# Optimization experiments

Measured on AMD Instinct MI355X. Metric: run time of the kernel, lower is better.

The kernel has to match this reference:

```python
import jax, jax.numpy as jnp
import numpy as np

T, H, O, L = 8192, 512, 256, 5  # num_frames, hidden(=input), output, num_layers


def setup_inputs() -> dict:
    key = jax.random.key(0)
    ks = jax.random.split(key, 16)
    s = 1.0 / np.sqrt(H)
    def w(k, shape):
        return jax.random.uniform(k, shape, jnp.float32, -s, s)
    d = {"x": jax.random.normal(ks[0], (T, H), jnp.float32)}
    names = ["Wz", "Uz", "Wr", "Ur", "Wh", "Uh"]
    for i, n in enumerate(names):
        d[n] = w(ks[1 + i], (L, H, H))
        d["b" + n] = w(ks[7 + i], (L, H))
    d["fcW"] = w(ks[13], (O, H))
    d["fcb"] = w(ks[14], (O,))
    return d


def _gru_forward(x, Wz, Uz, Wr, Ur, Wh, Uh, bWz, bUz, bWr, bUr, bWh, bUh):
    # x: [T, H]; weights: [L, H, H]; biases: [L, H]
    nl, hs = Wz.shape[0], Wz.shape[1]
    h0 = jnp.zeros((nl, hs), x.dtype)

    def time_step(h, x_t):  # h: [L, H], x_t: [H]
        def layer_step(x_in, p):
            wz, uz, wr, ur, wh, uh, bwz, buz, bwr, bur, bwh, buh, h_prev = p
            z = jax.nn.sigmoid(x_in @ wz.T + bwz + h_prev @ uz.T + buz)
            r = jax.nn.sigmoid(x_in @ wr.T + bwr + h_prev @ ur.T + bur)
            h_tilde = jnp.tanh(x_in @ wh.T + bwh + (r * h_prev) @ uh.T + buh)
            h_new = (1.0 - z) * h_prev + z * h_tilde
            return h_new, h_new  # next layer's input is this layer's hidden

        _, h_new = jax.lax.scan(
            layer_step, x_t,
            (Wz, Uz, Wr, Ur, Wh, Uh, bWz, bUz, bWr, bUr, bWh, bUh, h))
        return h_new, h_new[-1]  # carry new stacked state, emit top-layer h

    h_final, outs = jax.lax.scan(time_step, h0, x)
    return outs, h_final  # outs: [T, H], h_final: [L, H]


def reference(x, Wz, Uz, Wr, Ur, Wh, Uh, bWz, bUz, bWr, bUr, bWh, bUh, fcW, fcb):
    outs, h_final = _gru_forward(x, Wz, Uz, Wr, Ur, Wh, Uh,
                                 bWz, bUz, bWr, bUr, bWh, bUh)
    out = outs @ fcW.T + fcb  # [T, O]
    return out, h_final
```

## Files before the change

kernel.cpp:

```cpp
#include <hip/hip_runtime.h>
#include <math.h>

#define TT 8192
#define HH 512
#define LL 5
#define OO 256
#define GG 32
#define NR 16
#define NTHR 256
#define RB 64
#define HOT 4u
#define CAP_TAG 2000000u
#define CAP_PRG 200000u

typedef unsigned long long u64;
typedef unsigned u32;


__device__ __forceinline__ float wred(float v) {
#pragma unroll
  for (int off = 32; off > 0; off >>= 1) v += __shfl_xor(v, off, 64);
  return v;
}

__device__ __forceinline__ float sigm(float v) {
  return 1.0f / (1.0f + expf(-v));
}

__device__ __forceinline__ u64 ldA(const u64* p) {
  return __hip_atomic_load((u64*)p, __ATOMIC_RELAXED, __HIP_MEMORY_SCOPE_AGENT);
}
__device__ __forceinline__ void stA(u64* p, u64 v) {
  __hip_atomic_store(p, v, __ATOMIC_RELAXED, __HIP_MEMORY_SCOPE_AGENT);
}
__device__ __forceinline__ u64 pack(u32 tag, float v) {
  return ((u64)tag << 32) | (u64)__float_as_uint(v);
}


__global__ void init_ws(u32* __restrict__ p, int n) {
  int stride = gridDim.x * blockDim.x;
  for (int i = blockIdx.x * blockDim.x + threadIdx.x; i < n; i += stride) p[i] = 0u;
}


__launch_bounds__(NTHR, 1)
__global__ void gru_pipeline(
    const float* __restrict__ x,
    const float* __restrict__ Wz, const float* __restrict__ bWz,
    const float* __restrict__ Uz, const float* __restrict__ bUz,
    const float* __restrict__ Wr, const float* __restrict__ bWr,
    const float* __restrict__ Ur, const float* __restrict__ bUr,
    const float* __restrict__ Wh, const float* __restrict__ bWh,
    const float* __restrict__ Uh, const float* __restrict__ bUh,
    u64* __restrict__ hring,
    u64* __restrict__ rring,
    float* __restrict__ htop,
    u32* __restrict__ prog,
    float* __restrict__ dout)
{
  const int blk = blockIdx.x;
  const int l = blk / GG;
  const int g = blk % GG;
  const bool ltop = (l == LL - 1);
  const int i0 = g * NR;

  const int tid = threadIdx.x;
  const int wave = tid >> 6;
  const int lane = tid & 63;
  const int j0 = lane * 8;
  const int j = tid * 2;

  __shared__ float xs[HH];
  __shared__ float hs[HH];
  __shared__ float rh[HH];
  __shared__ int dead_s;
  volatile int* dead = &dead_s;
  if (tid == 0) dead_s = 0;

  float wz[4][8], uz[4][8], wr[4][8], ur[4][8], wh[4][8], uh[4][8];
  float bz[4], br[4], bh[4];
  int rowg[4];
#pragma unroll
  for (int k = 0; k < 4; ++k) {
    const int i = i0 + wave + 4 * k;
    rowg[k] = i;
    const size_t ro = ((size_t)l * HH + i) * HH + j0;
    *(float4*)&wz[k][0] = *(const float4*)(Wz + ro);
    *(float4*)&wz[k][4] = *(const float4*)(Wz + ro + 4);
    *(float4*)&uz[k][0] = *(const float4*)(Uz + ro);
    *(float4*)&uz[k][4] = *(const float4*)(Uz + ro + 4);
    *(float4*)&wr[k][0] = *(const float4*)(Wr + ro);
    *(float4*)&wr[k][4] = *(const float4*)(Wr + ro + 4);
    *(float4*)&ur[k][0] = *(const float4*)(Ur + ro);
    *(float4*)&ur[k][4] = *(const float4*)(Ur + ro + 4);
    *(float4*)&wh[k][0] = *(const float4*)(Wh + ro);
    *(float4*)&wh[k][4] = *(const float4*)(Wh + ro + 4);
    *(float4*)&uh[k][0] = *(const float4*)(Uh + ro);
    *(float4*)&uh[k][4] = *(const float4*)(Uh + ro + 4);
    bz[k] = bWz[l * HH + i] + bUz[l * HH + i];
    br[k] = bWr[l * HH + i] + bUr[l * HH + i];
    bh[k] = bWh[l * HH + i] + bUh[l * HH + i];
  }

  u64* my_h = hring + (size_t)l * RB * HH;
  const u64* up_h = hring + (size_t)(l > 0 ? l - 1 : 0) * RB * HH;
  u64* my_r = rring + (size_t)l * 2 * HH;
  u32* my_prog = prog + l * GG + g;
  u32* dn_prog = prog + (l < LL - 1 ? l + 1 : l) * GG;

  float zreg[4], awreg[4], hpown[4];
#pragma unroll
  for (int k = 0; k < 4; ++k) { zreg[k] = 0.f; awreg[k] = 0.f; hpown[k] = 0.f; }

  __syncthreads();

  for (int t = 0; t < TT; ++t) {
    {
      const u64* sx = (l > 0) ? up_h + (size_t)(t & (RB - 1)) * HH + j : (const u64*)0;
      const u64* sh = (t > 0) ? my_h + (size_t)((t - 1) & (RB - 1)) * HH + j : (const u64*)0;
      const u32 tagx = (u32)(t + 1), tagh = (u32)t;
      u64 ax = 0, bx = 0, ah = 0, bh2 = 0;
      if (sx) { ax = ldA(sx); bx = ldA(sx + 1); }
      if (sh) { ah = ldA(sh); bh2 = ldA(sh + 1); }
      u32 n = 0;
      for (;;) {
        const bool badx = sx && (((u32)(ax >> 32) != tagx) || ((u32)(bx >> 32) != tagx));
        const bool badh = sh && (((u32)(ah >> 32) != tagh) || ((u32)(bh2 >> 32) != tagh));
        if (!badx && !badh) break;
        if (++n > HOT) {
          __builtin_amdgcn_s_sleep(2);
          if (*dead) break;
          if (n > CAP_TAG) { *dead = 1; break; }
        }
        if (badx) { ax = ldA(sx); bx = ldA(sx + 1); }
        if (badh) { ah = ldA(sh); bh2 = ldA(sh + 1); }
      }
      if (sx) { xs[j] = __uint_as_float((u32)ax); xs[j + 1] = __uint_as_float((u32)bx); }
      else {
        const float2 v = *(const float2*)&x[(size_t)t * HH + j];
        xs[j] = v.x; xs[j + 1] = v.y;
      }
      if (sh) { hs[j] = __uint_as_float((u32)ah); hs[j + 1] = __uint_as_float((u32)bh2); }
      else { hs[j] = 0.f; hs[j + 1] = 0.f; }
    }
    if (wave == 3 && !ltop && t >= RB && lane < GG) {
      const u32 need = (u32)(t - RB + 1);
      u32 n = 0;
      while (__hip_atomic_load(&dn_prog[lane], __ATOMIC_RELAXED,
                               __HIP_MEMORY_SCOPE_AGENT) < need) {
        if (*dead) break;
        if (++n > CAP_PRG) { *dead = 1; break; }
        __builtin_amdgcn_s_sleep(16);
      }
    }
    __syncthreads();

    if (tid == 0)
      __hip_atomic_store(my_prog, (u32)(t + 1), __ATOMIC_RELAXED, __HIP_MEMORY_SCOPE_AGENT);

    float xv[8], hv[8];
    *(float4*)&xv[0] = *(const float4*)&xs[j0];
    *(float4*)&xv[4] = *(const float4*)&xs[j0 + 4];
    *(float4*)&hv[0] = *(const float4*)&hs[j0];
    *(float4*)&hv[4] = *(const float4*)&hs[j0 + 4];
#pragma unroll
    for (int k = 0; k < 4; ++k) hpown[k] = hs[rowg[k]];

    u64* hsl = my_h + (size_t)(t & (RB - 1)) * HH;

    if (t == 0) {
#pragma unroll
      for (int k = 0; k < 4; ++k) {
        float az = 0.f, aw = 0.f;
#pragma unroll
        for (int q = 0; q < 8; ++q) {
          az = fmaf(wz[k][q], xv[q], az);
          aw = fmaf(wh[k][q], xv[q], aw);
        }
        az = wred(az); aw = wred(aw);
        if (lane == 0) {
          const float hnew = sigm(az + bz[k]) * tanhf(aw + bh[k]);
          stA(&hsl[rowg[k]], pack(1u, hnew));
          if (ltop) htop[(size_t)0 * HH + rowg[k]] = hnew;
        }
      }
      __syncthreads();
      continue;
    }

    u64* rs = my_r + (size_t)(t & 1) * HH;
    const u32 tag1 = (u32)(t + 1);
#pragma unroll
    for (int k = 0; k < 4; ++k) {
      float ar = 0.f;
#pragma unroll
      for (int q = 0; q < 8; ++q) {
        ar = fmaf(wr[k][q], xv[q], ar);
        ar = fmaf(ur[k][q], hv[q], ar);
      }
      ar = wred(ar);
      if (lane == 0) stA(&rs[rowg[k]], pack(tag1, sigm(ar + br[k])));
    }

#pragma unroll
    for (int k = 0; k < 4; ++k) {
      float az = 0.f, aw = 0.f;
#pragma unroll
      for (int q = 0; q < 8; ++q) {
        az = fmaf(wz[k][q], xv[q], az);
        az = fmaf(uz[k][q], hv[q], az);
        aw = fmaf(wh[k][q], xv[q], aw);
      }
      az = wred(az); aw = wred(aw);
      if (lane == 0) {
        zreg[k] = sigm(az + bz[k]);
        awreg[k] = aw + bh[k];
      }
    }

    {
      const u64* s = rs + j;
      u64 a = ldA(s), b = ldA(s + 1);
      u32 n = 0;
      while ((u32)(a >> 32) != tag1 || (u32)(b >> 32) != tag1) {
        if (++n > HOT) {
          __builtin_amdgcn_s_sleep(2);
          if (*dead) break;
          if (n > CAP_TAG) { *dead = 1; break; }
        }
        if ((u32)(a >> 32) != tag1) a = ldA(s);
        if ((u32)(b >> 32) != tag1) b = ldA(s + 1);
      }
      rh[j]     = __uint_as_float((u32)a) * hs[j];
      rh[j + 1] = __uint_as_float((u32)b) * hs[j + 1];
    }
    __syncthreads();

    float rhv[8];
    *(float4*)&rhv[0] = *(const float4*)&rh[j0];
    *(float4*)&rhv[4] = *(const float4*)&rh[j0 + 4];

#pragma unroll
    for (int k = 0; k < 4; ++k) {
      float u = 0.f;
#pragma unroll
      for (int q = 0; q < 8; ++q) u = fmaf(uh[k][q], rhv[q], u);
      u = wred(u);
      if (lane == 0) {
        const float z = zreg[k];
        const float ht = tanhf(awreg[k] + u);
        const float hnew = (1.f - z) * hpown[k] + z * ht;
        stA(&hsl[rowg[k]], pack(tag1, hnew));
        if (ltop) htop[(size_t)t * HH + rowg[k]] = hnew;
        if (t == TT - 1) dout[(size_t)TT * OO + (size_t)l * HH + rowg[k]] = hnew;
      }
    }
  }
}


__launch_bounds__(256)
__global__ void fc_gemm(const float* __restrict__ A,
                        const float* __restrict__ W,
                        const float* __restrict__ bias,
                        float* __restrict__ C) {
  __shared__ float As[16][68];
  __shared__ float Ws[16][68];
  const int bm = blockIdx.x;
  const int bn = blockIdx.y;
  const int tid = threadIdx.x;
  const int tx = tid & 15;
  const int ty = tid >> 4;
  const int r = tid >> 2;
  const int kc = (tid & 3) * 4;
  float acc[4][4];
#pragma unroll
  for (int a = 0; a < 4; ++a)
#pragma unroll
    for (int b2 = 0; b2 < 4; ++b2) acc[a][b2] = 0.f;

  for (int k0 = 0; k0 < HH; k0 += 16) {
    const float4 a4 = *(const float4*)&A[(size_t)(bm * 64 + r) * HH + k0 + kc];
    const float4 w4 = *(const float4*)&W[(size_t)(bn * 64 + r) * HH + k0 + kc];
    __syncthreads();
    As[kc + 0][r] = a4.x; As[kc + 1][r] = a4.y; As[kc + 2][r] = a4.z; As[kc + 3][r] = a4.w;
    Ws[kc + 0][r] = w4.x; Ws[kc + 1][r] = w4.y; Ws[kc + 2][r] = w4.z; Ws[kc + 3][r] = w4.w;
    __syncthreads();
#pragma unroll
    for (int kk = 0; kk < 16; ++kk) {
      const float4 av = *(const float4*)&As[kk][ty * 4];
      const float4 wv = *(const float4*)&Ws[kk][tx * 4];
      const float avv[4] = {av.x, av.y, av.z, av.w};
      const float wvv[4] = {wv.x, wv.y, wv.z, wv.w};
#pragma unroll
      for (int a = 0; a < 4; ++a)
#pragma unroll
        for (int b2 = 0; b2 < 4; ++b2)
          acc[a][b2] = fmaf(avv[a], wvv[b2], acc[a][b2]);
    }
  }
#pragma unroll
  for (int a = 0; a < 4; ++a) {
    const int row = bm * 64 + ty * 4 + a;
#pragma unroll
    for (int b2 = 0; b2 < 4; ++b2) {
      const int col = bn * 64 + tx * 4 + b2;
      C[(size_t)row * OO + col] = acc[a][b2] + bias[col];
    }
  }
}


extern "C" void kernel_launch(void* const* d_in, const int* in_sizes, int n_in,
                              void* d_out, int out_size, void* d_ws, size_t ws_size,
                              hipStream_t stream) {
  const float* p[15];
  for (int i = 0; i < 15 && i < n_in; ++i) p[i] = (const float*)d_in[i];

  const float *x, *Wz, *bWz, *Uz, *bUz, *Wr, *bWr, *Ur, *bUr, *Wh, *bWh, *Uh, *bUh, *fcW, *fcb;
  x = p[0];
  if (in_sizes[2] == LL * HH) {
    Wz = p[1]; bWz = p[2]; Uz = p[3]; bUz = p[4];
    Wr = p[5]; bWr = p[6]; Ur = p[7]; bUr = p[8];
    Wh = p[9]; bWh = p[10]; Uh = p[11]; bUh = p[12];
  } else {
    Wz = p[1]; Uz = p[2]; Wr = p[3]; Ur = p[4]; Wh = p[5]; Uh = p[6];
    bWz = p[7]; bUz = p[8]; bWr = p[9]; bUr = p[10]; bWh = p[11]; bUh = p[12];
  }
  fcW = p[13]; fcb = p[14];

  u64* hring = (u64*)d_ws;
  u64* rring = hring + (size_t)LL * RB * HH;
  u32* prog = (u32*)(rring + (size_t)LL * 2 * HH);
  float* htop = (float*)(prog + (size_t)LL * GG);

  const int zero_u32 = (int)(((size_t)LL * RB * HH + (size_t)LL * 2 * HH) * 2 + LL * GG);
  init_ws<<<512, 256, 0, stream>>>((u32*)d_ws, zero_u32);

  gru_pipeline<<<LL * GG, NTHR, 0, stream>>>(
      x, Wz, bWz, Uz, bUz, Wr, bWr, Ur, bUr, Wh, bWh, Uh, bUh,
      hring, rring, htop, prog, (float*)d_out);

  fc_gemm<<<dim3(TT / 64, OO / 64), 256, 0, stream>>>(
      htop, fcW, fcb, (float*)d_out);
}
```

Before: 54.05 ms.

## Make each wave poll global rings directly and drop block-level barriers

Each wave now reads the tagged hidden-state and upper-layer values straight from the global rings with a strided per-lane layout, instead of staging them in shared memory behind __syncthreads. Progress counters are tracked per wave, and r*h_prev is computed by the owning lane before publishing, so consumers no longer multiply by h themselves. This removes two block barriers per timestep and the shared-memory round trip on the serial critical path. In exchange, every wave issues its own atomic polls, which multiplies global polling traffic.

```diff
diff --git a/kernel.cpp b/kernel.cpp
--- a/kernel.cpp
+++ b/kernel.cpp
@@ -6,12 +6,10 @@
 #define LL 5
 #define OO 256
 #define GG 32
-#define NR 16
 #define NTHR 256
 #define RB 64
-#define HOT 4u
-#define CAP_TAG 2000000u
-#define CAP_PRG 200000u
+#define CAP_TAG 4000000u
+#define CAP_PRG 4000000u
 
 typedef unsigned long long u64;
 typedef unsigned u32;
@@ -31,6 +29,12 @@
   return __hip_atomic_load((u64*)p, __ATOMIC_RELAXED, __HIP_MEMORY_SCOPE_AGENT);
 }
 __device__ __forceinline__ void stA(u64* p, u64 v) {
+  __hip_atomic_store(p, v, __ATOMIC_RELAXED, __HIP_MEMORY_SCOPE_AGENT);
+}
+__device__ __forceinline__ u32 ld32(const u32* p) {
+  return __hip_atomic_load((u32*)p, __ATOMIC_RELAXED, __HIP_MEMORY_SCOPE_AGENT);
+}
+__device__ __forceinline__ void st32(u32* p, u32 v) {
   __hip_atomic_store(p, v, __ATOMIC_RELAXED, __HIP_MEMORY_SCOPE_AGENT);
 }
 __device__ __forceinline__ u64 pack(u32 tag, float v) {
@@ -63,41 +67,30 @@
   const int l = blk / GG;
   const int g = blk % GG;
   const bool ltop = (l == LL - 1);
-  const int i0 = g * NR;
-
   const int tid = threadIdx.x;
   const int wave = tid >> 6;
   const int lane = tid & 63;
-  const int j0 = lane * 8;
-  const int j = tid * 2;
-
-  __shared__ float xs[HH];
-  __shared__ float hs[HH];
-  __shared__ float rh[HH];
+  const int i0 = g * 16 + wave * 4;
+
   __shared__ int dead_s;
   volatile int* dead = &dead_s;
   if (tid == 0) dead_s = 0;
 
   float wz[4][8], uz[4][8], wr[4][8], ur[4][8], wh[4][8], uh[4][8];
   float bz[4], br[4], bh[4];
-  int rowg[4];
 #pragma unroll
   for (int k = 0; k < 4; ++k) {
-    const int i = i0 + wave + 4 * k;
-    rowg[k] = i;
-    const size_t ro = ((size_t)l * HH + i) * HH + j0;
-    *(float4*)&wz[k][0] = *(const float4*)(Wz + ro);
-    *(float4*)&wz[k][4] = *(const float4*)(Wz + ro + 4);
-    *(float4*)&uz[k][0] = *(const float4*)(Uz + ro);
-    *(float4*)&uz[k][4] = *(const float4*)(Uz + ro + 4);
-    *(float4*)&wr[k][0] = *(const float4*)(Wr + ro);
-    *(float4*)&wr[k][4] = *(const float4*)(Wr + ro + 4);
-    *(float4*)&ur[k][0] = *(const float4*)(Ur + ro);
-    *(float4*)&ur[k][4] = *(const float4*)(Ur + ro + 4);
-    *(float4*)&wh[k][0] = *(const float4*)(Wh + ro);
-    *(float4*)&wh[k][4] = *(const float4*)(Wh + ro + 4);
-    *(float4*)&uh[k][0] = *(const float4*)(Uh + ro);
-    *(float4*)&uh[k][4] = *(const float4*)(Uh + ro + 4);
+    const int i = i0 + k;
+    const size_t ro = ((size_t)l * HH + i) * HH + lane;
+#pragma unroll
+    for (int q = 0; q < 8; ++q) {
+      wz[k][q] = Wz[ro + 64 * q];
+      uz[k][q] = Uz[ro + 64 * q];
+      wr[k][q] = Wr[ro + 64 * q];
+      ur[k][q] = Ur[ro + 64 * q];
+      wh[k][q] = Wh[ro + 64 * q];
+      uh[k][q] = Uh[ro + 64 * q];
+    }
     bz[k] = bWz[l * HH + i] + bUz[l * HH + i];
     br[k] = bWr[l * HH + i] + bUr[l * HH + i];
     bh[k] = bWh[l * HH + i] + bUh[l * HH + i];
@@ -106,66 +99,64 @@
   u64* my_h = hring + (size_t)l * RB * HH;
   const u64* up_h = hring + (size_t)(l > 0 ? l - 1 : 0) * RB * HH;
   u64* my_r = rring + (size_t)l * 2 * HH;
-  u32* my_prog = prog + l * GG + g;
-  u32* dn_prog = prog + (l < LL - 1 ? l + 1 : l) * GG;
-
-  float zreg[4], awreg[4], hpown[4];
-#pragma unroll
-  for (int k = 0; k < 4; ++k) { zreg[k] = 0.f; awreg[k] = 0.f; hpown[k] = 0.f; }
+  u32* my_prog = prog + ((size_t)l * GG + g) * 4 + wave;
+  const u32* dnp = prog + (size_t)(l < LL - 1 ? l + 1 : l) * GG * 4;
+
+  float hprev[4] = {0.f, 0.f, 0.f, 0.f};
 
   __syncthreads();
 
   for (int t = 0; t < TT; ++t) {
-    {
-      const u64* sx = (l > 0) ? up_h + (size_t)(t & (RB - 1)) * HH + j : (const u64*)0;
-      const u64* sh = (t > 0) ? my_h + (size_t)((t - 1) & (RB - 1)) * HH + j : (const u64*)0;
-      const u32 tagx = (u32)(t + 1), tagh = (u32)t;
-      u64 ax = 0, bx = 0, ah = 0, bh2 = 0;
-      if (sx) { ax = ldA(sx); bx = ldA(sx + 1); }
-      if (sh) { ah = ldA(sh); bh2 = ldA(sh + 1); }
-      u32 n = 0;
-      for (;;) {
-        const bool badx = sx && (((u32)(ax >> 32) != tagx) || ((u32)(bx >> 32) != tagx));
-        const bool badh = sh && (((u32)(ah >> 32) != tagh) || ((u32)(bh2 >> 32) != tagh));
-        if (!badx && !badh) break;
-        if (++n > HOT) {
-          __builtin_amdgcn_s_sleep(2);
-          if (*dead) break;
-          if (n > CAP_TAG) { *dead = 1; break; }
-        }
-        if (badx) { ax = ldA(sx); bx = ldA(sx + 1); }
-        if (badh) { ah = ldA(sh); bh2 = ldA(sh + 1); }
-      }
-      if (sx) { xs[j] = __uint_as_float((u32)ax); xs[j + 1] = __uint_as_float((u32)bx); }
-      else {
-        const float2 v = *(const float2*)&x[(size_t)t * HH + j];
-        xs[j] = v.x; xs[j + 1] = v.y;
-      }
-      if (sh) { hs[j] = __uint_as_float((u32)ah); hs[j + 1] = __uint_as_float((u32)bh2); }
-      else { hs[j] = 0.f; hs[j + 1] = 0.f; }
-    }
-    if (wave == 3 && !ltop && t >= RB && lane < GG) {
+    if (!ltop && t >= RB) {
       const u32 need = (u32)(t - RB + 1);
       u32 n = 0;
-      while (__hip_atomic_load(&dn_prog[lane], __ATOMIC_RELAXED,
-                               __HIP_MEMORY_SCOPE_AGENT) < need) {
+      while (ld32(dnp + lane) < need || ld32(dnp + 64 + lane) < need) {
+        __builtin_amdgcn_s_sleep(16);
         if (*dead) break;
         if (++n > CAP_PRG) { *dead = 1; break; }
-        __builtin_amdgcn_s_sleep(16);
-      }
-    }
-    __syncthreads();
-
-    if (tid == 0)
-      __hip_atomic_store(my_prog, (u32)(t + 1), __ATOMIC_RELAXED, __HIP_MEMORY_SCOPE_AGENT);
+      }
+    }
 
     float xv[8], hv[8];
-    *(float4*)&xv[0] = *(const float4*)&xs[j0];
-    *(float4*)&xv[4] = *(const float4*)&xs[j0 + 4];
-    *(float4*)&hv[0] = *(const float4*)&hs[j0];
-    *(float4*)&hv[4] = *(const float4*)&hs[j0 + 4];
-#pragma unroll
-    for (int k = 0; k < 4; ++k) hpown[k] = hs[rowg[k]];
+    {
+      const u64* sx = (l > 0) ? up_h + (size_t)(t & (RB - 1)) * HH : (const u64*)0;
+      const u64* sh = (t > 0) ? my_h + (size_t)((t - 1) & (RB - 1)) * HH : (const u64*)0;
+      const u32 tgx = (u32)(t + 1), tgh = (u32)t;
+      u64 vx[8], vh[8];
+      u32 mx = sx ? 0xFFu : 0u, mh = sh ? 0xFFu : 0u, n = 0;
+      while (mx | mh) {
+#pragma unroll
+        for (int q = 0; q < 8; ++q) if (mx & (1u << q)) vx[q] = ldA(sx + lane + 64 * q);
+#pragma unroll
+        for (int q = 0; q < 8; ++q) if (mh & (1u << q)) vh[q] = ldA(sh + lane + 64 * q);
+#pragma unroll
+        for (int q = 0; q < 8; ++q)
+          if ((mx & (1u << q)) && (u32)(vx[q] >> 32) == tgx) mx &= ~(1u << q);
+#pragma unroll
+        for (int q = 0; q < 8; ++q)
+          if ((mh & (1u << q)) && (u32)(vh[q] >> 32) == tgh) mh &= ~(1u << q);
+        if (!(mx | mh)) break;
+        __builtin_amdgcn_s_sleep(2);
+        if (*dead) break;
+        if (++n > CAP_TAG) { *dead = 1; break; }
+      }
+      if (sx) {
+#pragma unroll
+        for (int q = 0; q < 8; ++q) xv[q] = __uint_as_float((u32)vx[q]);
+      } else {
+#pragma unroll
+        for (int q = 0; q < 8; ++q) xv[q] = x[(size_t)t * HH + lane + 64 * q];
+      }
+      if (sh) {
+#pragma unroll
+        for (int q = 0; q < 8; ++q) hv[q] = __uint_as_float((u32)vh[q]);
+      } else {
+#pragma unroll
+        for (int q = 0; q < 8; ++q) hv[q] = 0.f;
+      }
+    }
+
+    if (lane == 0) st32(my_prog, (u32)(t + 1));
 
     u64* hsl = my_h + (size_t)(t & (RB - 1)) * HH;
 
@@ -181,16 +172,17 @@
         az = wred(az); aw = wred(aw);
         if (lane == 0) {
           const float hnew = sigm(az + bz[k]) * tanhf(aw + bh[k]);
-          stA(&hsl[rowg[k]], pack(1u, hnew));
-          if (ltop) htop[(size_t)0 * HH + rowg[k]] = hnew;
+          hprev[k] = hnew;
+          stA(&hsl[i0 + k], pack(1u, hnew));
+          if (ltop) htop[i0 + k] = hnew;
         }
       }
-      __syncthreads();
       continue;
     }
 
+    const u32 tg = (u32)(t + 1);
     u64* rs = my_r + (size_t)(t & 1) * HH;
-    const u32 tag1 = (u32)(t + 1);
+
 #pragma unroll
     for (int k = 0; k < 4; ++k) {
       float ar = 0.f;
@@ -200,9 +192,10 @@
         ar = fmaf(ur[k][q], hv[q], ar);
       }
       ar = wred(ar);
-      if (lane == 0) stA(&rs[rowg[k]], pack(tag1, sigm(ar + br[k])));
-    }
-
+      if (lane == 0) stA(&rs[i0 + k], pack(tg, sigm(ar + br[k]) * hprev[k]));
+    }
+
+    float zk[4], awk[4];
 #pragma unroll
     for (int k = 0; k < 4; ++k) {
       float az = 0.f, aw = 0.f;
@@ -213,33 +206,29 @@
         aw = fmaf(wh[k][q], xv[q], aw);
       }
       az = wred(az); aw = wred(aw);
-      if (lane == 0) {
-        zreg[k] = sigm(az + bz[k]);
-        awreg[k] = aw + bh[k];
-      }
-    }
-
+      zk[k] = sigm(az + bz[k]);
+      awk[k] = aw + bh[k];
+    }
+
+    float rhv[8];
     {
-      const u64* s = rs + j;
-      u64 a = ldA(s), b = ldA(s + 1);
-      u32 n = 0;
-      while ((u32)(a >> 32) != tag1 || (u32)(b >> 32) != tag1) {
-        if (++n > HOT) {
-          __builtin_amdgcn_s_sleep(2);
-          if (*dead) break;
-          if (n > CAP_TAG) { *dead = 1; break; }
-        }
-        if ((u32)(a >> 32) != tag1) a = ldA(s);
-        if ((u32)(b >> 32) != tag1) b = ldA(s + 1);
-      }
-      rh[j]     = __uint_as_float((u32)a) * hs[j];
-      rh[j + 1] = __uint_as_float((u32)b) * hs[j + 1];
-    }
-    __syncthreads();
-
-    float rhv[8];
-    *(float4*)&rhv[0] = *(const float4*)&rh[j0];
-    *(float4*)&rhv[4] = *(const float4*)&rh[j0 + 4];
+      const u64* s = rs;
+      u64 v[8];
+      u32 m = 0xFFu, n = 0;
+      for (;;) {
+#pragma unroll
+        for (int q = 0; q < 8; ++q) if (m & (1u << q)) v[q] = ldA(s + lane + 64 * q);
+#pragma unroll
+        for (int q = 0; q < 8; ++q)
+          if ((m & (1u << q)) && (u32)(v[q] >> 32) == tg) m &= ~(1u << q);
+        if (!m) break;
+        __builtin_amdgcn_s_sleep(2);
+        if (*dead) break;
+        if (++n > CAP_TAG) { *dead = 1; break; }
+      }
+#pragma unroll
+      for (int q = 0; q < 8; ++q) rhv[q] = __uint_as_float((u32)v[q]);
+    }
 
 #pragma unroll
     for (int k = 0; k < 4; ++k) {
@@ -248,12 +237,12 @@
       for (int q = 0; q < 8; ++q) u = fmaf(uh[k][q], rhv[q], u);
       u = wred(u);
       if (lane == 0) {
-        const float z = zreg[k];
-        const float ht = tanhf(awreg[k] + u);
-        const float hnew = (1.f - z) * hpown[k] + z * ht;
-        stA(&hsl[rowg[k]], pack(tag1, hnew));
-        if (ltop) htop[(size_t)t * HH + rowg[k]] = hnew;
-        if (t == TT - 1) dout[(size_t)TT * OO + (size_t)l * HH + rowg[k]] = hnew;
+        const float ht = tanhf(awk[k] + u);
+        const float hnew = (1.f - zk[k]) * hprev[k] + zk[k] * ht;
+        hprev[k] = hnew;
+        stA(&hsl[i0 + k], pack(tg, hnew));
+        if (ltop) htop[(size_t)t * HH + i0 + k] = hnew;
+        if (t == TT - 1) dout[(size_t)TT * OO + (size_t)l * HH + i0 + k] = hnew;
       }
     }
   }
@@ -333,9 +322,10 @@
   u64* hring = (u64*)d_ws;
   u64* rring = hring + (size_t)LL * RB * HH;
   u32* prog = (u32*)(rring + (size_t)LL * 2 * HH);
-  float* htop = (float*)(prog + (size_t)LL * GG);
-
-  const int zero_u32 = (int)(((size_t)LL * RB * HH + (size_t)LL * 2 * HH) * 2 + LL * GG);
+  float* htop = (float*)(prog + (size_t)LL * GG * 4);
+
+  const int zero_u32 = (int)(((size_t)LL * RB * HH + (size_t)LL * 2 * HH) * 2
+                             + (size_t)LL * GG * 4);
   init_ws<<<512, 256, 0, stream>>>((u32*)d_ws, zero_u32);
 
   gru_pipeline<<<LL * GG, NTHR, 0, stream>>>(
```

After: 61.34 ms. +13.5%, slower.
